# Kernel tuning notes

Hardware: AMD Instinct MI355X
Metric: run time of the kernel (lower is better)

## Reference

```python
import jax, jax.numpy as jnp
import numpy as np

B, D = 65536, 256

def setup_inputs() -> dict:
    key = jax.random.key(0)
    ks = jax.random.split(key, 8)
    return {
        "drug_cnn": jax.random.normal(ks[0], (B, D), dtype=jnp.float32),
        "drug_kg": jax.random.normal(ks[1], (B, D), dtype=jnp.float32),
        "w_aa": jax.random.normal(ks[2], (D, 1), dtype=jnp.float32),
        "w_ab": jax.random.normal(ks[3], (D, 1), dtype=jnp.float32),
        "w_ba": jax.random.normal(ks[4], (D, 1), dtype=jnp.float32),
        "w_bb": jax.random.normal(ks[5], (D, 1), dtype=jnp.float32),
        "d_cnn_bias": jax.random.normal(ks[6], (D, 1), dtype=jnp.float32),
        "d_kg_bias": jax.random.normal(ks[7], (D, 1), dtype=jnp.float32),
    }

def reference(drug_cnn, drug_kg, w_aa, w_ab, w_ba, w_bb, d_cnn_bias, d_kg_bias):
    # Variant 'KG-MTL-C' (the module default).
    # Original math: c_mat[b,i,j] = drug_cnn[b,i] * drug_kg[b,j]; note the
    # source has `c_mat_t = c_mat.view(...)` (NOT the permuted tensor), so
    # c_mat_t == c_mat and w_ab / w_bb also contract against drug_kg.
    #   out_cnn[b,i] = drug_cnn[b,i] * <drug_kg[b], w_aa + w_ab> + d_cnn_bias[i]
    #   out_kg [b,i] = drug_cnn[b,i] * <drug_kg[b], w_ba + w_bb> + d_kg_bias[i]
    # This collapses the [B,D,D] outer product into O(B*D) work (same values).
    s_cnn = drug_kg @ (w_aa + w_ab)              # [B, 1] per-row scalar
    s_kg = drug_kg @ (w_ba + w_bb)               # [B, 1]
    out_cnn = drug_cnn * s_cnn + d_cnn_bias[:, 0]  # [B, D] + [D] broadcast
    out_kg = drug_cnn * s_kg + d_kg_bias[:, 0]
    return (out_cnn, out_kg)
```

## Files before the change

### kernel.cpp

```cpp
#include <hip/hip_runtime.h>


constexpr int BN = 65536;
constexpr int DN = 256;

__global__ __launch_bounds__(256) void shared_unit_kernel(
    const float* __restrict__ drug_cnn,
    const float* __restrict__ drug_kg,
    const float* __restrict__ w_aa,
    const float* __restrict__ w_ab,
    const float* __restrict__ w_ba,
    const float* __restrict__ w_bb,
    const float* __restrict__ bias_cnn,
    const float* __restrict__ bias_kg,
    float* __restrict__ out)
{
    const int lane = threadIdx.x & 63;
    const int wid  = (blockIdx.x * blockDim.x + threadIdx.x) >> 6;
    const int nw   = (gridDim.x * blockDim.x) >> 6;
    const int j    = lane << 2;

    const float4 waa = *(const float4*)(w_aa + j);
    const float4 wab = *(const float4*)(w_ab + j);
    const float4 wba = *(const float4*)(w_ba + j);
    const float4 wbb = *(const float4*)(w_bb + j);
    const float4 wa  = make_float4(waa.x + wab.x, waa.y + wab.y, waa.z + wab.z, waa.w + wab.w);
    const float4 wb  = make_float4(wba.x + wbb.x, wba.y + wbb.y, wba.z + wbb.z, wba.w + wbb.w);
    const float4 bc  = *(const float4*)(bias_cnn + j);
    const float4 bk  = *(const float4*)(bias_kg + j);

    float* __restrict__ out_cnn = out;
    float* __restrict__ out_kg  = out + (size_t)BN * DN;

    for (int b = wid; b < BN; b += nw) {
        const size_t base = (size_t)b * DN + j;

        const float4 kg  = *(const float4*)(drug_kg  + base);
        const float4 cnn = *(const float4*)(drug_cnn + base);

        float sa = kg.x * wa.x + kg.y * wa.y + kg.z * wa.z + kg.w * wa.w;
        float sb = kg.x * wb.x + kg.y * wb.y + kg.z * wb.z + kg.w * wb.w;

        #pragma unroll
        for (int off = 1; off < 64; off <<= 1) {
            sa += __shfl_xor(sa, off);
            sb += __shfl_xor(sb, off);
        }

        const float4 oc = make_float4(cnn.x * sa + bc.x, cnn.y * sa + bc.y,
                                      cnn.z * sa + bc.z, cnn.w * sa + bc.w);
        const float4 ok = make_float4(cnn.x * sb + bk.x, cnn.y * sb + bk.y,
                                      cnn.z * sb + bk.z, cnn.w * sb + bk.w);

        *(float4*)(out_cnn + base) = oc;
        *(float4*)(out_kg  + base) = ok;
    }
}

extern "C" void kernel_launch(void* const* d_in, const int* in_sizes, int n_in,
                              void* d_out, int out_size, void* d_ws, size_t ws_size,
                              hipStream_t stream) {
    const float* drug_cnn = (const float*)d_in[0];
    const float* drug_kg  = (const float*)d_in[1];
    const float* w_aa     = (const float*)d_in[2];
    const float* w_ab     = (const float*)d_in[3];
    const float* w_ba     = (const float*)d_in[4];
    const float* w_bb     = (const float*)d_in[5];
    const float* b_cnn    = (const float*)d_in[6];
    const float* b_kg     = (const float*)d_in[7];
    float* out = (float*)d_out;

    dim3 grid(2048), block(256);
    hipLaunchKernelGGL(shared_unit_kernel, grid, block, 0, stream,
                       drug_cnn, drug_kg, w_aa, w_ab, w_ba, w_bb, b_cnn, b_kg, out);
}
```

Baseline: 46.63 us.

## Process two rows per wavefront with 8-wide lanes and nontemporal stores

New measurement: 54.78 us. 17.5% more time.

```diff
diff --git a/kernel.cpp b/kernel.cpp
--- a/kernel.cpp
+++ b/kernel.cpp
@@ -3,6 +3,8 @@
 
 constexpr int BN = 65536;
 constexpr int DN = 256;
+
+typedef float f32x4 __attribute__((ext_vector_type(4)));
 
 __global__ __launch_bounds__(256) void shared_unit_kernel(
     const float* __restrict__ drug_cnn,
@@ -15,45 +17,65 @@
     const float* __restrict__ bias_kg,
     float* __restrict__ out)
 {
-    const int lane = threadIdx.x & 63;
-    const int wid  = (blockIdx.x * blockDim.x + threadIdx.x) >> 6;
-    const int nw   = (gridDim.x * blockDim.x) >> 6;
-    const int j    = lane << 2;
+    const int lane    = threadIdx.x & 63;
+    const int half    = lane >> 5;
+    const int sublane = lane & 31;
+    const int j       = sublane << 3;
 
-    const float4 waa = *(const float4*)(w_aa + j);
-    const float4 wab = *(const float4*)(w_ab + j);
-    const float4 wba = *(const float4*)(w_ba + j);
-    const float4 wbb = *(const float4*)(w_bb + j);
-    const float4 wa  = make_float4(waa.x + wab.x, waa.y + wab.y, waa.z + wab.z, waa.w + wab.w);
-    const float4 wb  = make_float4(wba.x + wbb.x, wba.y + wbb.y, wba.z + wbb.z, wba.w + wbb.w);
-    const float4 bc  = *(const float4*)(bias_cnn + j);
-    const float4 bk  = *(const float4*)(bias_kg + j);
+    const int wid = (blockIdx.x * blockDim.x + threadIdx.x) >> 6;
+    const int nw  = (gridDim.x * blockDim.x) >> 6;
+
+    const f32x4 waa0 = *(const f32x4*)(w_aa + j);
+    const f32x4 waa1 = *(const f32x4*)(w_aa + j + 4);
+    const f32x4 wab0 = *(const f32x4*)(w_ab + j);
+    const f32x4 wab1 = *(const f32x4*)(w_ab + j + 4);
+    const f32x4 wba0 = *(const f32x4*)(w_ba + j);
+    const f32x4 wba1 = *(const f32x4*)(w_ba + j + 4);
+    const f32x4 wbb0 = *(const f32x4*)(w_bb + j);
+    const f32x4 wbb1 = *(const f32x4*)(w_bb + j + 4);
+
+    const f32x4 wa0 = waa0 + wab0;
+    const f32x4 wa1 = waa1 + wab1;
+    const f32x4 wb0 = wba0 + wbb0;
+    const f32x4 wb1 = wba1 + wbb1;
+
+    const f32x4 bc0 = *(const f32x4*)(bias_cnn + j);
+    const f32x4 bc1 = *(const f32x4*)(bias_cnn + j + 4);
+    const f32x4 bk0 = *(const f32x4*)(bias_kg + j);
+    const f32x4 bk1 = *(const f32x4*)(bias_kg + j + 4);
 
     float* __restrict__ out_cnn = out;
     float* __restrict__ out_kg  = out + (size_t)BN * DN;
 
-    for (int b = wid; b < BN; b += nw) {
+    for (int p = wid; p < BN / 2; p += nw) {
+        const int b = (p << 1) + half;
         const size_t base = (size_t)b * DN + j;
 
-        const float4 kg  = *(const float4*)(drug_kg  + base);
-        const float4 cnn = *(const float4*)(drug_cnn + base);
+        const f32x4 kg0 = *(const f32x4*)(drug_kg  + base);
+        const f32x4 kg1 = *(const f32x4*)(drug_kg  + base + 4);
+        const f32x4 cn0 = *(const f32x4*)(drug_cnn + base);
+        const f32x4 cn1 = *(const f32x4*)(drug_cnn + base + 4);
 
-        float sa = kg.x * wa.x + kg.y * wa.y + kg.z * wa.z + kg.w * wa.w;
-        float sb = kg.x * wb.x + kg.y * wb.y + kg.z * wb.z + kg.w * wb.w;
+        float sa = kg0.x * wa0.x + kg0.y * wa0.y + kg0.z * wa0.z + kg0.w * wa0.w
+                 + kg1.x * wa1.x + kg1.y * wa1.y + kg1.z * wa1.z + kg1.w * wa1.w;
+        float sb = kg0.x * wb0.x + kg0.y * wb0.y + kg0.z * wb0.z + kg0.w * wb0.w
+                 + kg1.x * wb1.x + kg1.y * wb1.y + kg1.z * wb1.z + kg1.w * wb1.w;
 
         #pragma unroll
-        for (int off = 1; off < 64; off <<= 1) {
+        for (int off = 1; off < 32; off <<= 1) {
             sa += __shfl_xor(sa, off);
             sb += __shfl_xor(sb, off);
         }
 
-        const float4 oc = make_float4(cnn.x * sa + bc.x, cnn.y * sa + bc.y,
-                                      cnn.z * sa + bc.z, cnn.w * sa + bc.w);
-        const float4 ok = make_float4(cnn.x * sb + bk.x, cnn.y * sb + bk.y,
-                                      cnn.z * sb + bk.z, cnn.w * sb + bk.w);
+        const f32x4 oc0 = cn0 * sa + bc0;
+        const f32x4 oc1 = cn1 * sa + bc1;
+        const f32x4 ok0 = cn0 * sb + bk0;
+        const f32x4 ok1 = cn1 * sb + bk1;
 
-        *(float4*)(out_cnn + base) = oc;
-        *(float4*)(out_kg  + base) = ok;
+        __builtin_nontemporal_store(oc0, (f32x4*)(out_cnn + base));
+        __builtin_nontemporal_store(oc1, (f32x4*)(out_cnn + base + 4));
+        __builtin_nontemporal_store(ok0, (f32x4*)(out_kg + base));
+        __builtin_nontemporal_store(ok1, (f32x4*)(out_kg + base + 4));
     }
 }
 
```
